# Kernel optimization log

Measured on AMD Instinct MI355X. Metric: run time of the kernel, lower is better.

Reference implementation:

```python
import jax, jax.numpy as jnp
import numpy as np

H, HK, D = 16, 4, 128          # query heads, kv heads, head_dim
HID, INTER = 2048, 8192        # hidden_size, intermediate_size
L, N_UND = 4096, 3072          # total packed len (sum(sample_lens)), num und tokens
SAMPLE_LENS = [2048, 2048]
EPS = 1e-6


def rmsnorm(x, w, eps=EPS):
    v = jnp.mean(jnp.square(x), axis=-1, keepdims=True)
    return x * jax.lax.rsqrt(v + eps) * w


def setup_inputs() -> dict:
    key = jax.random.key(0)
    ks = jax.random.split(key, 12)
    x = jax.random.normal(ks[0], (N_UND, HID), jnp.float32)
    und_idx = jnp.sort(jax.random.permutation(ks[1], L)[:N_UND]).astype(jnp.int64)
    # RoPE tables (source computes RoPE but its attention consumes pre-RoPE tensors)
    pos = jnp.arange(L, dtype=jnp.float32)
    inv_freq = 1.0 / (10000.0 ** (jnp.arange(0, D, 2, dtype=jnp.float32) / D))
    ang = pos[:, None] * inv_freq[None, :]
    cos = jnp.concatenate([jnp.cos(ang), jnp.cos(ang)], axis=-1)
    sin = jnp.concatenate([jnp.sin(ang), jnp.sin(ang)], axis=-1)
    # block-diagonal causal mask over packed sequence (one causal block per sample)
    offs = np.cumsum([0] + SAMPLE_LENS)
    m = np.zeros((L, L), dtype=bool)
    for a, b in zip(offs[:-1], offs[1:]):
        m[a:b, a:b] = np.tril(np.ones((b - a, b - a), dtype=bool))
    mask = jnp.asarray(m)
    w = lambda k, shape: jax.random.normal(k, shape, jnp.float32) * 0.02
    return dict(
        packed_sequence=x, und_idx=und_idx, cos=cos, sin=sin, mask=mask,
        Wq=w(ks[2], (H * D, HID)), bq=w(ks[3], (H * D,)),
        Wk=w(ks[4], (HK * D, HID)), bk=w(ks[5], (HK * D,)),
        Wv=w(ks[6], (HK * D, HID)), bv=w(ks[7], (HK * D,)),
        Wo=w(ks[8], (HID, H * D)),
        q_norm_w=jnp.ones((D,), jnp.float32), k_norm_w=jnp.ones((D,), jnp.float32),
        ln1_w=jnp.ones((HID,), jnp.float32), ln2_w=jnp.ones((HID,), jnp.float32),
        Wg=w(ks[9], (INTER, HID)), Wu=w(ks[10], (INTER, HID)), Wd=w(ks[11], (HID, INTER)),
    )


def reference(packed_sequence, und_idx, cos, sin, mask, Wq, bq, Wk, bk, Wv, bv, Wo,
              q_norm_w, k_norm_w, ln1_w, ln2_w, Wg, Wu, Wd):
    G = H // HK  # num_key_value_groups
    resid = packed_sequence
    x = rmsnorm(packed_sequence, ln1_w)
    # projections on und tokens only, then scatter into zero-initialized packed tensors
    q = (x @ Wq.T + bq).reshape(-1, H, D)
    k = (x @ Wk.T + bk).reshape(-1, HK, D)
    v = (x @ Wv.T + bv).reshape(-1, HK, D)
    Q = jnp.zeros((L, H, D), x.dtype).at[und_idx].set(q)
    K = jnp.zeros((L, HK, D), x.dtype).at[und_idx].set(k)
    V = jnp.zeros((L, HK, D), x.dtype).at[und_idx].set(v)
    # QK RMSNorm (zero rows stay zero, matching scatter-of-normed-und-rows)
    Q = rmsnorm(Q, q_norm_w)
    K = rmsnorm(K, k_norm_w)
    # NOTE: the source applies apply_rotary_pos_emb(Q, K, cos, sin) but both attention
    # branches consume the pre-RoPE normed tensors, so RoPE has no effect; we mirror that.
    Kx = jnp.repeat(K, G, axis=1)  # [L, H, D] GQA expand (each kv head repeated G times)
    Vx = jnp.repeat(V, G, axis=1)
    scores = jnp.einsum('qhd,khd->hqk', Q, Kx) / jnp.sqrt(jnp.asarray(D, x.dtype))
    scores = jnp.where(mask[None], scores, jnp.finfo(scores.dtype).min)
    attn = jax.nn.softmax(scores, axis=-1)
    ctx = jnp.einsum('hqk,khd->qhd', attn, Vx).reshape(L, H * D)
    attn_out = ctx[und_idx] @ Wo.T
    h = resid + attn_out
    y = rmsnorm(h, ln2_w)
    mlp = (jax.nn.silu(y @ Wg.T) * (y @ Wu.T)) @ Wd.T
    return h + mlp
```

## Files before the change

### kernel.cpp

```cpp
#include <hip/hip_runtime.h>
#include <math.h>


#define NU     3072
#define LPACK  4096
#define HIDN   2048
#define QKV_LD 3072
#define EPSF   1e-6f

typedef unsigned short u16;
typedef unsigned int   u32;
typedef __attribute__((ext_vector_type(8)))  __bf16 bf16x8;
typedef __attribute__((ext_vector_type(4)))  float  f32x4;
typedef __attribute__((ext_vector_type(16))) float  f32x16;

union FRAG { uint4 q; u16 u[8]; bf16x8 b; };

__device__ __forceinline__ u16 f2bf(float f) {
    u32 u = __float_as_uint(f);
    u32 r = (u + 0x7fffu + ((u >> 16) & 1u)) >> 16;
    return (u16)r;
}
__device__ __forceinline__ float bf2f(u16 h) {
    return __uint_as_float(((u32)h) << 16);
}
__device__ __forceinline__ void gload_lds16(const u16* g, u16* lds) {
    __builtin_amdgcn_global_load_lds(
        (const __attribute__((address_space(1))) u32*)g,
        (__attribute__((address_space(3))) u32*)lds, 16, 0, 0);
}


__global__ __launch_bounds__(256) void inv_init_kernel(int* __restrict__ inv) {
    inv[blockIdx.x * 256 + threadIdx.x] = -1;
}
__global__ __launch_bounds__(256) void inv_set_kernel(const int* __restrict__ und,
                                                      int* __restrict__ inv) {
    int i = blockIdx.x * 256 + threadIdx.x;
    inv[und[i]] = i;
}


__global__ __launch_bounds__(256) void cvt_bf16_kernel(const float* __restrict__ in,
                                                       u16* __restrict__ out, int n8) {
    int idx = blockIdx.x * 256 + threadIdx.x;
    int stride = gridDim.x * 256;
    for (int i = idx; i < n8; i += stride) {
        float4 a = *(const float4*)(in + (size_t)i * 8);
        float4 b = *(const float4*)(in + (size_t)i * 8 + 4);
        FRAG f;
        f.u[0] = f2bf(a.x); f.u[1] = f2bf(a.y); f.u[2] = f2bf(a.z); f.u[3] = f2bf(a.w);
        f.u[4] = f2bf(b.x); f.u[5] = f2bf(b.y); f.u[6] = f2bf(b.z); f.u[7] = f2bf(b.w);
        *(uint4*)(out + (size_t)i * 8) = f.q;
    }
}


__global__ __launch_bounds__(256) void rmsnorm_bf16_kernel(const float* __restrict__ in,
                                                           const float* __restrict__ w,
                                                           u16* __restrict__ out) {
    int row = blockIdx.x;
    const float4* p = (const float4*)(in + (size_t)row * HIDN);
    float4 a = p[threadIdx.x * 2];
    float4 b = p[threadIdx.x * 2 + 1];
    float ss = a.x*a.x + a.y*a.y + a.z*a.z + a.w*a.w
             + b.x*b.x + b.y*b.y + b.z*b.z + b.w*b.w;
    #pragma unroll
    for (int off = 32; off > 0; off >>= 1) ss += __shfl_xor(ss, off, 64);
    __shared__ float red[4];
    if ((threadIdx.x & 63) == 0) red[threadIdx.x >> 6] = ss;
    __syncthreads();
    float tot = red[0] + red[1] + red[2] + red[3];
    float sc  = rsqrtf(tot * (1.0f / HIDN) + EPSF);
    const float4* wp = (const float4*)w;
    float4 w0 = wp[threadIdx.x * 2], w1 = wp[threadIdx.x * 2 + 1];
    FRAG f;
    f.u[0] = f2bf(a.x*sc*w0.x); f.u[1] = f2bf(a.y*sc*w0.y);
    f.u[2] = f2bf(a.z*sc*w0.z); f.u[3] = f2bf(a.w*sc*w0.w);
    f.u[4] = f2bf(b.x*sc*w1.x); f.u[5] = f2bf(b.y*sc*w1.y);
    f.u[6] = f2bf(b.z*sc*w1.z); f.u[7] = f2bf(b.w*sc*w1.w);
    *(uint4*)(out + (size_t)row * HIDN + threadIdx.x * 8) = f.q;
}


__global__ __launch_bounds__(64) void qnorm_kernel(u16* __restrict__ qkv,
                                                   const float* __restrict__ w) {
    int i = blockIdx.x, h = blockIdx.y, t = threadIdx.x;
    u16* p = qkv + (size_t)i * QKV_LD + h * 128 + t * 2;
    u32 pr = *(u32*)p;
    float x0 = bf2f((u16)(pr & 0xffff)), x1 = bf2f((u16)(pr >> 16));
    float ss = x0*x0 + x1*x1;
    #pragma unroll
    for (int off = 32; off > 0; off >>= 1) ss += __shfl_xor(ss, off, 64);
    float sc = rsqrtf(ss * (1.0f / 128.f) + EPSF);
    float2 wv = *(const float2*)(w + t * 2);
    u32 res = (u32)f2bf(x0*sc*wv.x) | ((u32)f2bf(x1*sc*wv.y) << 16);
    *(u32*)p = res;
}


__global__ __launch_bounds__(64) void scatter_kv_kernel(const u16* __restrict__ qkvb,
                                                        const int* __restrict__ inv,
                                                        const float* __restrict__ knw,
                                                        u16* __restrict__ Kb,
                                                        u16* __restrict__ Vb) {
    int l = blockIdx.x, hkk = blockIdx.y, t = threadIdx.x;
    int i = inv[l];
    size_t off = (size_t)l * 512 + hkk * 128 + t * 2;
    if (i < 0) {
        *(u32*)(Kb + off) = 0u;
        *(u32*)(Vb + off) = 0u;
        return;
    }
    const u16* kp = qkvb + (size_t)i * QKV_LD + 2048 + hkk * 128 + t * 2;
    u32 kv = *(const u32*)kp;
    float k0 = bf2f((u16)(kv & 0xffff)), k1 = bf2f((u16)(kv >> 16));
    float ss = k0*k0 + k1*k1;
    #pragma unroll
    for (int off2 = 32; off2 > 0; off2 >>= 1) ss += __shfl_xor(ss, off2, 64);
    float sc = rsqrtf(ss * (1.0f / 128.f) + EPSF);
    float2 wv = *(const float2*)(knw + t * 2);
    u32 res = (u32)f2bf(k0*sc*wv.x) | ((u32)f2bf(k1*sc*wv.y) << 16);
    *(u32*)(Kb + off) = res;
    const u16* vp = qkvb + (size_t)i * QKV_LD + 2560 + hkk * 128 + t * 2;
    *(u32*)(Vb + off) = *(const u32*)vp;
}


template <int MODE>
__global__ __launch_bounds__(256, 2) void gemm_bf16_kernel(
        const u16* __restrict__ A, int lda,
        const u16* __restrict__ B0, const u16* __restrict__ B1, const u16* __restrict__ B2,
        int n1, int n2, int ldb,
        const float* __restrict__ bias0, const float* __restrict__ bias1,
        const float* __restrict__ bias2,
        const float* __restrict__ addend,
        void* __restrict__ Cout, int ldc, int K)
{
    __shared__ u16 As[128 * 64];
    __shared__ u16 Bs[128 * 64];
    const int tid = threadIdx.x;
    const int w = tid >> 6, lane = tid & 63;
    const int m0 = blockIdx.y * 128, n0 = blockIdx.x * 128;
    const u16* Bp; const float* bias; int nb;
    if (n0 < n1)      { Bp = B0; bias = bias0; nb = n0; }
    else if (n0 < n2) { Bp = B1; bias = bias1; nb = n0 - n1; }
    else              { Bp = B2; bias = bias2; nb = n0 - n2; }
    const int wr = w >> 1, wc = w & 1;
    const int cl = lane & 15, kg = lane >> 4;

    f32x4 acc[4][4];
    #pragma unroll
    for (int i = 0; i < 4; ++i)
        #pragma unroll
        for (int j = 0; j < 4; ++j)
            #pragma unroll
            for (int r = 0; r < 4; ++r) acc[i][j][r] = 0.f;

    for (int k0 = 0; k0 < K; k0 += 64) {
        #pragma unroll
        for (int j = 0; j < 4; ++j) {
            int slot = j * 256 + tid;
            int row = slot >> 3, jp = slot & 7;
            int j2 = jp ^ (row & 7);
            gload_lds16(A + (size_t)(m0 + row) * lda + k0 + j2 * 8,
                        &As[(j * 256 + w * 64) * 8]);
        }
        #pragma unroll
        for (int j = 0; j < 4; ++j) {
            int slot = j * 256 + tid;
            int row = slot >> 3, jp = slot & 7;
            int j2 = jp ^ (row & 7);
            gload_lds16(Bp + (size_t)(nb + row) * ldb + k0 + j2 * 8,
                        &Bs[(j * 256 + w * 64) * 8]);
        }
        __syncthreads();
        #pragma unroll
        for (int ks = 0; ks < 2; ++ks) {
            FRAG af[4], bfr[4];
            #pragma unroll
            for (int mi = 0; mi < 4; ++mi) {
                int row = wr * 64 + mi * 16 + cl;
                int dblk = ks * 4 + kg;
                af[mi].q = *(const uint4*)&As[row * 64 + ((dblk ^ (row & 7)) * 8)];
            }
            #pragma unroll
            for (int ni = 0; ni < 4; ++ni) {
                int row = wc * 64 + ni * 16 + cl;
                int dblk = ks * 4 + kg;
                bfr[ni].q = *(const uint4*)&Bs[row * 64 + ((dblk ^ (row & 7)) * 8)];
            }
            #pragma unroll
            for (int mi = 0; mi < 4; ++mi)
                #pragma unroll
                for (int ni = 0; ni < 4; ++ni)
                    acc[mi][ni] = __builtin_amdgcn_mfma_f32_16x16x32_bf16(
                        af[mi].b, bfr[ni].b, acc[mi][ni], 0, 0, 0);
        }
        __syncthreads();
    }
    #pragma unroll
    for (int mi = 0; mi < 4; ++mi) {
        #pragma unroll
        for (int ni = 0; ni < 4; ++ni) {
            int gcol = n0 + wc * 64 + ni * 16 + cl;
            float bv = 0.f;
            if (MODE == 0) bv = bias[nb + wc * 64 + ni * 16 + cl];
            #pragma unroll
            for (int r = 0; r < 4; ++r) {
                int grow = m0 + wr * 64 + mi * 16 + kg * 4 + r;
                float v = acc[mi][ni][r] + bv;
                if (MODE == 0) {
                    ((u16*)Cout)[(size_t)grow * ldc + gcol] = f2bf(v);
                } else {
                    v += addend[(size_t)grow * ldc + gcol];
                    ((float*)Cout)[(size_t)grow * ldc + gcol] = v;
                }
            }
        }
    }
}


__global__ __launch_bounds__(256, 2) void gemm_gateup_bf16_kernel(
        const u16* __restrict__ A,
        const u16* __restrict__ Bg, const u16* __restrict__ Bu,
        u16* __restrict__ act, int ldc)
{
    __shared__ u16 As[128 * 64];
    __shared__ u16 Gs[128 * 64];
    __shared__ u16 Us[128 * 64];
    const int tid = threadIdx.x;
    const int w = tid >> 6, lane = tid & 63;
    const int m0 = blockIdx.y * 128, n0 = blockIdx.x * 128;
    const int wr = w >> 1, wc = w & 1;
    const int cl = lane & 15, kg = lane >> 4;

    f32x4 ag[4][4], au[4][4];
    #pragma unroll
    for (int i = 0; i < 4; ++i)
        #pragma unroll
        for (int j = 0; j < 4; ++j)
            #pragma unroll
            for (int r = 0; r < 4; ++r) { ag[i][j][r] = 0.f; au[i][j][r] = 0.f; }

    for (int k0 = 0; k0 < HIDN; k0 += 64) {
        #pragma unroll
        for (int j = 0; j < 4; ++j) {
            int slot = j * 256 + tid;
            int row = slot >> 3, jp = slot & 7;
            int j2 = jp ^ (row & 7);
            gload_lds16(A + (size_t)(m0 + row) * HIDN + k0 + j2 * 8,
                        &As[(j * 256 + w * 64) * 8]);
            gload_lds16(Bg + (size_t)(n0 + row) * HIDN + k0 + j2 * 8,
                        &Gs[(j * 256 + w * 64) * 8]);
            gload_lds16(Bu + (size_t)(n0 + row) * HIDN + k0 + j2 * 8,
                        &Us[(j * 256 + w * 64) * 8]);
        }
        __syncthreads();
        #pragma unroll
        for (int ks = 0; ks < 2; ++ks) {
            FRAG af[4], gf[4], uf[4];
            #pragma unroll
            for (int mi = 0; mi < 4; ++mi) {
                int row = wr * 64 + mi * 16 + cl;
                int dblk = ks * 4 + kg;
                af[mi].q = *(const uint4*)&As[row * 64 + ((dblk ^ (row & 7)) * 8)];
            }
            #pragma unroll
            for (int ni = 0; ni < 4; ++ni) {
                int row = wc * 64 + ni * 16 + cl;
                int dblk = ks * 4 + kg;
                gf[ni].q = *(const uint4*)&Gs[row * 64 + ((dblk ^ (row & 7)) * 8)];
                uf[ni].q = *(const uint4*)&Us[row * 64 + ((dblk ^ (row & 7)) * 8)];
            }
            #pragma unroll
            for (int mi = 0; mi < 4; ++mi)
                #pragma unroll
                for (int ni = 0; ni < 4; ++ni) {
                    ag[mi][ni] = __builtin_amdgcn_mfma_f32_16x16x32_bf16(
                        af[mi].b, gf[ni].b, ag[mi][ni], 0, 0, 0);
                    au[mi][ni] = __builtin_amdgcn_mfma_f32_16x16x32_bf16(
                        af[mi].b, uf[ni].b, au[mi][ni], 0, 0, 0);
                }
        }
        __syncthreads();
    }
    #pragma unroll
    for (int mi = 0; mi < 4; ++mi) {
        #pragma unroll
        for (int ni = 0; ni < 4; ++ni) {
            int gcol = n0 + wc * 64 + ni * 16 + cl;
            #pragma unroll
            for (int r = 0; r < 4; ++r) {
                int grow = m0 + wr * 64 + mi * 16 + kg * 4 + r;
                float g = ag[mi][ni][r], u = au[mi][ni][r];
                float s = g / (1.f + __expf(-g));
                act[(size_t)grow * ldc + gcol] = f2bf(s * u);
            }
        }
    }
}


__global__ __launch_bounds__(256, 2) void attn_mfma_kernel(
        const u16* __restrict__ qkv,
        const u16* __restrict__ Kb,
        const u16* __restrict__ Vb,
        const int* __restrict__ und,
        u16* __restrict__ ctxb)
{
    const int h = blockIdx.y, hk = h >> 2;
    const int i0 = blockIdx.x * 128;
    const int tid = threadIdx.x;
    const int w = tid >> 6, lane = tid & 63;
    const int ql = lane & 31, hi = lane >> 5;

    __shared__ u16  Kt[32 * 128];
    __shared__ u16  Vt[128 * 40];
    __shared__ float Ot[4][32][36];

    const int iq  = i0 + w * 32 + ql;
    const int pqv = und[iq];
    const int rsv = pqv & ~2047;
    const int kend_w = __shfl(pqv, 31, 64);
    const int kbeg_w = __shfl(pqv, 0, 64) & ~2047;
    const int kbeg_b = und[i0] & ~2047;
    const int kend_b = und[i0 + 127];

    FRAG qf[8];
    const u16* qbase = qkv + (size_t)iq * QKV_LD + h * 128;
    #pragma unroll
    for (int ds = 0; ds < 8; ++ds)
        qf[ds].q = *(const uint4*)(qbase + ds * 16 + hi * 8);

    f32x16 Oa[4];
    #pragma unroll
    for (int dg = 0; dg < 4; ++dg)
        #pragma unroll
        for (int r = 0; r < 16; ++r) Oa[dg][r] = 0.f;
    float m_run = -1e30f, l_run = 0.f;
    const float SCALE = 0.08838834764831845f;

    for (int k0 = kbeg_b; k0 <= kend_b; k0 += 32) {
        #pragma unroll
        for (int j = 0; j < 2; ++j) {
            int sb = (j * 4 + w) * 64;
            int slot = sb + lane;
            int r = slot >> 4, jp = slot & 15;
            int jj = jp ^ (r & 15);
            gload_lds16(Kb + (size_t)(k0 + r) * 512 + hk * 128 + jj * 8, &Kt[sb * 8]);
        }
        {
            int kp = tid & 15, d0 = (tid >> 4) * 8;
            const u16* v0 = Vb + (size_t)(k0 + kp * 2) * 512 + hk * 128 + d0;
            FRAG r0, r1;
            r0.q = *(const uint4*)v0;
            r1.q = *(const uint4*)(v0 + 512);
            #pragma unroll
            for (int i = 0; i < 8; ++i) {
                u32 val = (u32)r0.u[i] | ((u32)r1.u[i] << 16);
                *(u32*)&Vt[(d0 + i) * 40 + kp * 2] = val;
            }
        }
        __syncthreads();
        if (k0 + 31 >= kbeg_w && k0 <= kend_w) {
            f32x16 st;
            #pragma unroll
            for (int r = 0; r < 16; ++r) st[r] = 0.f;
            #pragma unroll
            for (int ds = 0; ds < 8; ++ds) {
                FRAG kf;
                kf.q = *(const uint4*)&Kt[ql * 128 + (((ds * 2 + hi) ^ (ql & 15)) * 8)];
                st = __builtin_amdgcn_mfma_f32_32x32x16_bf16(kf.b, qf[ds].b, st, 0, 0, 0);
            }
            float p[16];
            float mloc = -1e30f;
            #pragma unroll
            for (int r = 0; r < 16; ++r) {
                int key = k0 + (r & 3) + ((r >> 2) << 3) + (hi << 2);
                float s = (key >= rsv && key <= pqv) ? st[r] * SCALE : -1e30f;
                p[r] = s;
                mloc = fmaxf(mloc, s);
            }
            float mfull = fmaxf(mloc, __shfl_xor(mloc, 32, 64));
            float mnew = fmaxf(m_run, mfull);
            float corr = __expf(m_run - mnew);
            float psum = 0.f;
            #pragma unroll
            for (int r = 0; r < 16; ++r) {
                float e = (p[r] > -1e29f) ? __expf(p[r] - mnew) : 0.f;
                p[r] = e; psum += e;
            }
            psum += __shfl_xor(psum, 32, 64);
            l_run = l_run * corr + psum;
            if (__any(mnew > m_run)) {
                #pragma unroll
                for (int r = 0; r < 16; ++r) {
                    float cr = __shfl(corr, (r & 3) + ((r >> 2) << 3) + (hi << 2), 64);
                    #pragma unroll
                    for (int dg = 0; dg < 4; ++dg) Oa[dg][r] *= cr;
                }
            }
            m_run = mnew;
            u32 pa[2][4];
            #pragma unroll
            for (int s = 0; s < 2; ++s) {
                #pragma unroll
                for (int t = 0; t < 2; ++t) {
                    u32 a = (u32)f2bf(p[8*s + 2*t]) | ((u32)f2bf(p[8*s + 2*t + 1]) << 16);
                    u32 b = (u32)f2bf(p[8*s + 4 + 2*t]) | ((u32)f2bf(p[8*s + 4 + 2*t + 1]) << 16);
                    asm volatile("v_permlane32_swap_b32 %0, %1" : "+v"(a), "+v"(b));
                    pa[s][t] = a; pa[s][t + 2] = b;
                }
            }
            #pragma unroll
            for (int s = 0; s < 2; ++s) {
                FRAG pau;
                pau.q = make_uint4(pa[s][0], pa[s][1], pa[s][2], pa[s][3]);
                #pragma unroll
                for (int dg = 0; dg < 4; ++dg) {
                    FRAG vf;
                    vf.q = *(const uint4*)&Vt[(dg * 32 + ql) * 40 + s * 16 + hi * 8];
                    Oa[dg] = __builtin_amdgcn_mfma_f32_32x32x16_bf16(pau.b, vf.b, Oa[dg], 0, 0, 0);
                }
            }
        }
        __syncthreads();
    }
    float linv = 1.f / l_run;
    #pragma unroll
    for (int dg = 0; dg < 4; ++dg) {
        #pragma unroll
        for (int r = 0; r < 16; ++r)
            Ot[w][(r & 3) + ((r >> 2) << 3) + (hi << 2)][ql] = Oa[dg][r];
        __syncthreads();
        float4 v0 = *(const float4*)&Ot[w][ql][hi * 16 + 0];
        float4 v1 = *(const float4*)&Ot[w][ql][hi * 16 + 4];
        float4 v2 = *(const float4*)&Ot[w][ql][hi * 16 + 8];
        float4 v3 = *(const float4*)&Ot[w][ql][hi * 16 + 12];
        FRAG a, b;
        a.u[0] = f2bf(v0.x * linv); a.u[1] = f2bf(v0.y * linv);
        a.u[2] = f2bf(v0.z * linv); a.u[3] = f2bf(v0.w * linv);
        a.u[4] = f2bf(v1.x * linv); a.u[5] = f2bf(v1.y * linv);
        a.u[6] = f2bf(v1.z * linv); a.u[7] = f2bf(v1.w * linv);
        b.u[0] = f2bf(v2.x * linv); b.u[1] = f2bf(v2.y * linv);
        b.u[2] = f2bf(v2.z * linv); b.u[3] = f2bf(v2.w * linv);
        b.u[4] = f2bf(v3.x * linv); b.u[5] = f2bf(v3.y * linv);
        b.u[6] = f2bf(v3.z * linv); b.u[7] = f2bf(v3.w * linv);
        u16* dst = ctxb + (size_t)(i0 + w * 32 + ql) * HIDN + h * 128 + dg * 32 + hi * 16;
        *(uint4*)dst = a.q;
        *(uint4*)(dst + 8) = b.q;
        __syncthreads();
    }
}


extern "C" void kernel_launch(void* const* d_in, const int* in_sizes, int n_in,
                              void* d_out, int out_size, void* d_ws, size_t ws_size,
                              hipStream_t stream) {
    const float* x    = (const float*)d_in[0];
    const int*   und  = (const int*)d_in[1];
    const float* Wq  = (const float*)d_in[5];
    const float* bq  = (const float*)d_in[6];
    const float* Wk  = (const float*)d_in[7];
    const float* bk  = (const float*)d_in[8];
    const float* Wv  = (const float*)d_in[9];
    const float* bv  = (const float*)d_in[10];
    const float* Wo  = (const float*)d_in[11];
    const float* qnw = (const float*)d_in[12];
    const float* knw = (const float*)d_in[13];
    const float* ln1 = (const float*)d_in[14];
    const float* ln2 = (const float*)d_in[15];
    const float* Wg  = (const float*)d_in[16];
    const float* Wu  = (const float*)d_in[17];
    const float* Wd  = (const float*)d_in[18];
    float* out = (float*)d_out;

    char* W = (char*)d_ws;
    u16* WqB = (u16*)(W + 0);
    u16* WkB = (u16*)(W + 8388608);
    u16* WvB = (u16*)(W + 10485760);
    u16* WoB = (u16*)(W + 12582912);
    u16* WgB = (u16*)(W + 20971520);
    u16* WuB = (u16*)(W + 54525952);
    u16* WdB = (u16*)(W + 88080384);
    char* R1 = W + 121634816;
    u16* qkvb = (u16*)R1;
    u16* ctxb = (u16*)(R1 + 18874368);
    u16* acth = (u16*)R1;
    float* hbuf = (float*)(W + 153092096);
    u16* xnb = (u16*)(W + 178257920);
    u16* Kbf = xnb;
    u16* Vbf = (u16*)(W + 178257920 + 4194304);
    u16* ynb = xnb;
    int* inv = (int*)(W + 190840832);

    const int BIG = 1 << 30;

    inv_init_kernel<<<16, 256, 0, stream>>>(inv);
    inv_set_kernel<<<12, 256, 0, stream>>>(und, inv);

    cvt_bf16_kernel<<<2048, 256, 0, stream>>>(Wq, WqB, 524288);
    cvt_bf16_kernel<<<512,  256, 0, stream>>>(Wk, WkB, 131072);
    cvt_bf16_kernel<<<512,  256, 0, stream>>>(Wv, WvB, 131072);
    cvt_bf16_kernel<<<2048, 256, 0, stream>>>(Wo, WoB, 524288);
    cvt_bf16_kernel<<<4096, 256, 0, stream>>>(Wg, WgB, 2097152);
    cvt_bf16_kernel<<<4096, 256, 0, stream>>>(Wu, WuB, 2097152);
    cvt_bf16_kernel<<<4096, 256, 0, stream>>>(Wd, WdB, 2097152);

    rmsnorm_bf16_kernel<<<NU, 256, 0, stream>>>(x, ln1, xnb);
    gemm_bf16_kernel<0><<<dim3(24, 24), 256, 0, stream>>>(
        xnb, 2048, WqB, WkB, WvB, 2048, 2560, 2048,
        bq, bk, bv, nullptr, qkvb, QKV_LD, 2048);
    qnorm_kernel<<<dim3(NU, 16), 64, 0, stream>>>(qkvb, qnw);
    scatter_kv_kernel<<<dim3(LPACK, 4), 64, 0, stream>>>(qkvb, inv, knw, Kbf, Vbf);
    attn_mfma_kernel<<<dim3(24, 16), 256, 0, stream>>>(qkvb, Kbf, Vbf, und, ctxb);
    gemm_bf16_kernel<1><<<dim3(16, 24), 256, 0, stream>>>(
        ctxb, 2048, WoB, WoB, WoB, BIG, BIG, 2048,
        nullptr, nullptr, nullptr, x, hbuf, 2048, 2048);
    rmsnorm_bf16_kernel<<<NU, 256, 0, stream>>>(hbuf, ln2, ynb);
    gemm_gateup_bf16_kernel<<<dim3(32, 24), 256, 0, stream>>>(
        ynb, WgB, WuB, acth, 4096);
    gemm_bf16_kernel<1><<<dim3(16, 24), 256, 0, stream>>>(
        acth, 4096, WdB, WdB, WdB, BIG, BIG, 8192,
        nullptr, nullptr, nullptr, hbuf, out, 2048, 4096);
    gemm_gateup_bf16_kernel<<<dim3(32, 24), 256, 0, stream>>>(
        ynb, WgB + (size_t)4096 * 2048, WuB + (size_t)4096 * 2048, acth, 4096);
    gemm_bf16_kernel<1><<<dim3(16, 24), 256, 0, stream>>>(
        acth, 4096, WdB + 4096, WdB, WdB, BIG, BIG, 8192,
        nullptr, nullptr, nullptr, out, out, 2048, 4096);
}
```

Baseline: 735.0 us.

## Split attention key range across wave pairs and merge softmax partials in LDS

The attention kernel now handles 64 queries per block instead of 128, with two wave pairs each walking half of the key tiles (split-K style). The partial max, sum and output of the two halves are merged through shared memory before the bf16 write, and the grid is doubled. This targets poor occupancy and load imbalance from the causal key range, since only 384 blocks previously ran long serial loops on 256 CUs. It also raises wave priority around the MFMA sections. The cost is a larger LDS footprint (36KB), an extra merge step, and K/V tiles that are no longer shared across all four waves.

```diff
diff --git a/kernel.cpp b/kernel.cpp
--- a/kernel.cpp
+++ b/kernel.cpp
@@ -311,22 +311,30 @@
         u16* __restrict__ ctxb)
 {
     const int h = blockIdx.y, hk = h >> 2;
-    const int i0 = blockIdx.x * 128;
+    const int i0 = blockIdx.x * 64;
     const int tid = threadIdx.x;
     const int w = tid >> 6, lane = tid & 63;
     const int ql = lane & 31, hi = lane >> 5;
-
-    __shared__ u16  Kt[32 * 128];
-    __shared__ u16  Vt[128 * 40];
-    __shared__ float Ot[4][32][36];
-
-    const int iq  = i0 + w * 32 + ql;
+    const int qsub = w & 1, kh = w >> 1;
+    const int tid2 = qsub * 64 + lane;
+
+    __shared__ __align__(16) unsigned char SM[36864];
+    u16*  Kt = (u16*)SM;
+    u16*  Vt = (u16*)(SM + 16384);
+    float* mM = (float*)SM;
+    float* mL = (float*)(SM + 512);
+    float* Om = (float*)(SM + 1024);
+    float* Ot = (float*)(SM + 9216);
+
+    const int iq  = i0 + qsub * 32 + ql;
     const int pqv = und[iq];
     const int rsv = pqv & ~2047;
     const int kend_w = __shfl(pqv, 31, 64);
     const int kbeg_w = __shfl(pqv, 0, 64) & ~2047;
     const int kbeg_b = und[i0] & ~2047;
-    const int kend_b = und[i0 + 127];
+    const int kend_b = und[i0 + 63];
+    const int ntiles = ((kend_b - kbeg_b) >> 5) + 1;
+    const int nhalf  = (ntiles + 1) >> 1;
 
     FRAG qf[8];
     const u16* qbase = qkv + (size_t)iq * QKV_LD + h * 128;
@@ -342,38 +350,48 @@
     float m_run = -1e30f, l_run = 0.f;
     const float SCALE = 0.08838834764831845f;
 
-    for (int k0 = kbeg_b; k0 <= kend_b; k0 += 32) {
-        #pragma unroll
-        for (int j = 0; j < 2; ++j) {
-            int sb = (j * 4 + w) * 64;
-            int slot = sb + lane;
-            int r = slot >> 4, jp = slot & 15;
-            int jj = jp ^ (r & 15);
-            gload_lds16(Kb + (size_t)(k0 + r) * 512 + hk * 128 + jj * 8, &Kt[sb * 8]);
-        }
-        {
-            int kp = tid & 15, d0 = (tid >> 4) * 8;
-            const u16* v0 = Vb + (size_t)(k0 + kp * 2) * 512 + hk * 128 + d0;
-            FRAG r0, r1;
-            r0.q = *(const uint4*)v0;
-            r1.q = *(const uint4*)(v0 + 512);
-            #pragma unroll
-            for (int i = 0; i < 8; ++i) {
-                u32 val = (u32)r0.u[i] | ((u32)r1.u[i] << 16);
-                *(u32*)&Vt[(d0 + i) * 40 + kp * 2] = val;
-            }
-        }
-        __syncthreads();
-        if (k0 + 31 >= kbeg_w && k0 <= kend_w) {
+    for (int it = 0; it < nhalf; ++it) {
+        const int t = kh ? (nhalf + it) : it;
+        const bool active = t < ntiles;
+        const int k0 = kbeg_b + (active ? t : 0) * 32;
+        if (active) {
+            #pragma unroll
+            for (int j = 0; j < 4; ++j) {
+                int slot = j * 128 + tid2;
+                int r = slot >> 4, jp = slot & 15;
+                int jj = jp ^ (r & 15);
+                gload_lds16(Kb + (size_t)(k0 + r) * 512 + hk * 128 + jj * 8,
+                            &Kt[kh * 4096 + (j * 128 + qsub * 64) * 8]);
+            }
+            int kp = tid2 & 15, d0 = (tid2 >> 4) * 8;
+            #pragma unroll
+            for (int h2 = 0; h2 < 2; ++h2) {
+                int dd = d0 + h2 * 64;
+                const u16* v0 = Vb + (size_t)(k0 + kp * 2) * 512 + hk * 128 + dd;
+                FRAG r0, r1;
+                r0.q = *(const uint4*)v0;
+                r1.q = *(const uint4*)(v0 + 512);
+                #pragma unroll
+                for (int i = 0; i < 8; ++i) {
+                    u32 val = (u32)r0.u[i] | ((u32)r1.u[i] << 16);
+                    *(u32*)&Vt[kh * 5120 + (dd + i) * 40 + kp * 2] = val;
+                }
+            }
+        }
+        __syncthreads();
+        if (active && k0 + 31 >= kbeg_w && k0 <= kend_w) {
             f32x16 st;
             #pragma unroll
             for (int r = 0; r < 16; ++r) st[r] = 0.f;
+            __builtin_amdgcn_s_setprio(1);
             #pragma unroll
             for (int ds = 0; ds < 8; ++ds) {
                 FRAG kf;
-                kf.q = *(const uint4*)&Kt[ql * 128 + (((ds * 2 + hi) ^ (ql & 15)) * 8)];
+                kf.q = *(const uint4*)&Kt[kh * 4096 + ql * 128 +
+                                          (((ds * 2 + hi) ^ (ql & 15)) * 8)];
                 st = __builtin_amdgcn_mfma_f32_32x32x16_bf16(kf.b, qf[ds].b, st, 0, 0, 0);
             }
+            __builtin_amdgcn_s_setprio(0);
             float p[16];
             float mloc = -1e30f;
             #pragma unroll
@@ -407,13 +425,14 @@
             #pragma unroll
             for (int s = 0; s < 2; ++s) {
                 #pragma unroll
-                for (int t = 0; t < 2; ++t) {
-                    u32 a = (u32)f2bf(p[8*s + 2*t]) | ((u32)f2bf(p[8*s + 2*t + 1]) << 16);
-                    u32 b = (u32)f2bf(p[8*s + 4 + 2*t]) | ((u32)f2bf(p[8*s + 4 + 2*t + 1]) << 16);
+                for (int t2 = 0; t2 < 2; ++t2) {
+                    u32 a = (u32)f2bf(p[8*s + 2*t2]) | ((u32)f2bf(p[8*s + 2*t2 + 1]) << 16);
+                    u32 b = (u32)f2bf(p[8*s + 4 + 2*t2]) | ((u32)f2bf(p[8*s + 4 + 2*t2 + 1]) << 16);
                     asm volatile("v_permlane32_swap_b32 %0, %1" : "+v"(a), "+v"(b));
-                    pa[s][t] = a; pa[s][t + 2] = b;
+                    pa[s][t2] = a; pa[s][t2 + 2] = b;
                 }
             }
+            __builtin_amdgcn_s_setprio(1);
             #pragma unroll
             for (int s = 0; s < 2; ++s) {
                 FRAG pau;
@@ -421,36 +440,70 @@
                 #pragma unroll
                 for (int dg = 0; dg < 4; ++dg) {
                     FRAG vf;
-                    vf.q = *(const uint4*)&Vt[(dg * 32 + ql) * 40 + s * 16 + hi * 8];
+                    vf.q = *(const uint4*)&Vt[kh * 5120 + (dg * 32 + ql) * 40 +
+                                              s * 16 + hi * 8];
                     Oa[dg] = __builtin_amdgcn_mfma_f32_32x32x16_bf16(pau.b, vf.b, Oa[dg], 0, 0, 0);
                 }
             }
-        }
-        __syncthreads();
-    }
-    float linv = 1.f / l_run;
+            __builtin_amdgcn_s_setprio(0);
+        }
+        __syncthreads();
+    }
+
+    if (hi == 0) {
+        mM[(kh * 2 + qsub) * 32 + ql] = m_run;
+        mL[(kh * 2 + qsub) * 32 + ql] = l_run;
+    }
+    __syncthreads();
+    float m0 = mM[qsub * 32 + ql],      l0 = mL[qsub * 32 + ql];
+    float m1 = mM[64 + qsub * 32 + ql], l1 = mL[64 + qsub * 32 + ql];
+    float mstar = fmaxf(m0, m1);
+    float f0 = __expf(m0 - mstar), f1 = __expf(m1 - mstar);
+    float lstar = f0 * l0 + f1 * l1;
+    float f_own = kh ? f1 : f0;
+    #pragma unroll
+    for (int r = 0; r < 16; ++r) {
+        float fr = __shfl(f_own, (r & 3) + ((r >> 2) << 3) + (hi << 2), 64);
+        #pragma unroll
+        for (int dg = 0; dg < 4; ++dg) Oa[dg][r] *= fr;
+    }
+    float linv = 1.f / lstar;
+
     #pragma unroll
     for (int dg = 0; dg < 4; ++dg) {
-        #pragma unroll
-        for (int r = 0; r < 16; ++r)
-            Ot[w][(r & 3) + ((r >> 2) << 3) + (hi << 2)][ql] = Oa[dg][r];
-        __syncthreads();
-        float4 v0 = *(const float4*)&Ot[w][ql][hi * 16 + 0];
-        float4 v1 = *(const float4*)&Ot[w][ql][hi * 16 + 4];
-        float4 v2 = *(const float4*)&Ot[w][ql][hi * 16 + 8];
-        float4 v3 = *(const float4*)&Ot[w][ql][hi * 16 + 12];
-        FRAG a, b;
-        a.u[0] = f2bf(v0.x * linv); a.u[1] = f2bf(v0.y * linv);
-        a.u[2] = f2bf(v0.z * linv); a.u[3] = f2bf(v0.w * linv);
-        a.u[4] = f2bf(v1.x * linv); a.u[5] = f2bf(v1.y * linv);
-        a.u[6] = f2bf(v1.z * linv); a.u[7] = f2bf(v1.w * linv);
-        b.u[0] = f2bf(v2.x * linv); b.u[1] = f2bf(v2.y * linv);
-        b.u[2] = f2bf(v2.z * linv); b.u[3] = f2bf(v2.w * linv);
-        b.u[4] = f2bf(v3.x * linv); b.u[5] = f2bf(v3.y * linv);
-        b.u[6] = f2bf(v3.z * linv); b.u[7] = f2bf(v3.w * linv);
-        u16* dst = ctxb + (size_t)(i0 + w * 32 + ql) * HIDN + h * 128 + dg * 32 + hi * 16;
-        *(uint4*)dst = a.q;
-        *(uint4*)(dst + 8) = b.q;
+        if (kh == 1) {
+            #pragma unroll
+            for (int r = 0; r < 16; ++r) {
+                int crow = (r & 3) + ((r >> 2) << 3) + (hi << 2);
+                Om[qsub * 1024 + crow * 32 + ql] = Oa[dg][r];
+            }
+        }
+        __syncthreads();
+        if (kh == 0) {
+            #pragma unroll
+            for (int r = 0; r < 16; ++r) {
+                int crow = (r & 3) + ((r >> 2) << 3) + (hi << 2);
+                float v = Oa[dg][r] + Om[qsub * 1024 + crow * 32 + ql];
+                Ot[qsub * 1152 + crow * 36 + ql] = v;
+            }
+            float4 v0 = *(const float4*)&Ot[qsub * 1152 + ql * 36 + hi * 16 + 0];
+            float4 v1 = *(const float4*)&Ot[qsub * 1152 + ql * 36 + hi * 16 + 4];
+            float4 v2 = *(const float4*)&Ot[qsub * 1152 + ql * 36 + hi * 16 + 8];
+            float4 v3 = *(const float4*)&Ot[qsub * 1152 + ql * 36 + hi * 16 + 12];
+            FRAG a, b;
+            a.u[0] = f2bf(v0.x * linv); a.u[1] = f2bf(v0.y * linv);
+            a.u[2] = f2bf(v0.z * linv); a.u[3] = f2bf(v0.w * linv);
+            a.u[4] = f2bf(v1.x * linv); a.u[5] = f2bf(v1.y * linv);
+            a.u[6] = f2bf(v1.z * linv); a.u[7] = f2bf(v1.w * linv);
+            b.u[0] = f2bf(v2.x * linv); b.u[1] = f2bf(v2.y * linv);
+            b.u[2] = f2bf(v2.z * linv); b.u[3] = f2bf(v2.w * linv);
+            b.u[4] = f2bf(v3.x * linv); b.u[5] = f2bf(v3.y * linv);
+            b.u[6] = f2bf(v3.z * linv); b.u[7] = f2bf(v3.w * linv);
+            u16* dst = ctxb + (size_t)(i0 + qsub * 32 + ql) * HIDN + h * 128 +
+                       dg * 32 + hi * 16;
+            *(uint4*)dst = a.q;
+            *(uint4*)(dst + 8) = b.q;
+        }
         __syncthreads();
     }
 }
@@ -515,7 +568,7 @@
         bq, bk, bv, nullptr, qkvb, QKV_LD, 2048);
     qnorm_kernel<<<dim3(NU, 16), 64, 0, stream>>>(qkvb, qnw);
     scatter_kv_kernel<<<dim3(LPACK, 4), 64, 0, stream>>>(qkvb, inv, knw, Kbf, Vbf);
-    attn_mfma_kernel<<<dim3(24, 16), 256, 0, stream>>>(qkvb, Kbf, Vbf, und, ctxb);
+    attn_mfma_kernel<<<dim3(48, 16), 256, 0, stream>>>(qkvb, Kbf, Vbf, und, ctxb);
     gemm_bf16_kernel<1><<<dim3(16, 24), 256, 0, stream>>>(
         ctxb, 2048, WoB, WoB, WoB, BIG, BIG, 2048,
         nullptr, nullptr, nullptr, x, hbuf, 2048, 2048);
```

Measured after the change: 751.4 us. +2.2%, slower.

## Double-buffer K/V tiles in attention and batch weight conversions into one launch

Applied to the files above, without the earlier changes.

The attention kernel now prefetches the next K tile into a second LDS buffer via global_load_lds and holds the next V tile in registers while the current tile is computed. This drops one barrier per iteration and hides load latency behind the MFMA work, and s_setprio raises wave priority around the MFMA sections. Shared memory is merged into one aliased byte buffer, so the epilogue reuses the K/V space. The seven weight-conversion launches become one 2D-grid kernel that reads per-segment arguments, cutting launch overhead at the cost of a fixed 1024-block grid per segment.

```diff
diff --git a/kernel.cpp b/kernel.cpp
--- a/kernel.cpp
+++ b/kernel.cpp
@@ -41,16 +41,25 @@
 }
 
 
-__global__ __launch_bounds__(256) void cvt_bf16_kernel(const float* __restrict__ in,
-                                                       u16* __restrict__ out, int n8) {
+struct CvtArgs {
+    const float* src[7];
+    u16*         dst[7];
+    int          n8[7];
+};
+
+__global__ __launch_bounds__(256) void cvt_all_kernel(CvtArgs a) {
+    int seg = blockIdx.y;
+    const float* in = a.src[seg];
+    u16* out = a.dst[seg];
+    int n8 = a.n8[seg];
     int idx = blockIdx.x * 256 + threadIdx.x;
     int stride = gridDim.x * 256;
     for (int i = idx; i < n8; i += stride) {
-        float4 a = *(const float4*)(in + (size_t)i * 8);
-        float4 b = *(const float4*)(in + (size_t)i * 8 + 4);
+        float4 va = *(const float4*)(in + (size_t)i * 8);
+        float4 vb = *(const float4*)(in + (size_t)i * 8 + 4);
         FRAG f;
-        f.u[0] = f2bf(a.x); f.u[1] = f2bf(a.y); f.u[2] = f2bf(a.z); f.u[3] = f2bf(a.w);
-        f.u[4] = f2bf(b.x); f.u[5] = f2bf(b.y); f.u[6] = f2bf(b.z); f.u[7] = f2bf(b.w);
+        f.u[0] = f2bf(va.x); f.u[1] = f2bf(va.y); f.u[2] = f2bf(va.z); f.u[3] = f2bf(va.w);
+        f.u[4] = f2bf(vb.x); f.u[5] = f2bf(vb.y); f.u[6] = f2bf(vb.z); f.u[7] = f2bf(vb.w);
         *(uint4*)(out + (size_t)i * 8) = f.q;
     }
 }
@@ -316,9 +325,10 @@
     const int w = tid >> 6, lane = tid & 63;
     const int ql = lane & 31, hi = lane >> 5;
 
-    __shared__ u16  Kt[32 * 128];
-    __shared__ u16  Vt[128 * 40];
-    __shared__ float Ot[4][32][36];
+    __shared__ __align__(16) unsigned char SM[36864];
+    u16*  Kt = (u16*)SM;
+    u16*  Vt = (u16*)(SM + 16384);
+    float* Ot = (float*)SM;
 
     const int iq  = i0 + w * 32 + ql;
     const int pqv = und[iq];
@@ -327,6 +337,7 @@
     const int kbeg_w = __shfl(pqv, 0, 64) & ~2047;
     const int kbeg_b = und[i0] & ~2047;
     const int kend_b = und[i0 + 127];
+    const int nt = ((kend_b - kbeg_b) >> 5) + 1;
 
     FRAG qf[8];
     const u16* qbase = qkv + (size_t)iq * QKV_LD + h * 128;
@@ -342,38 +353,61 @@
     float m_run = -1e30f, l_run = 0.f;
     const float SCALE = 0.08838834764831845f;
 
-    for (int k0 = kbeg_b; k0 <= kend_b; k0 += 32) {
+    const int kp = tid & 15, d0 = (tid >> 4) * 8;
+
+    FRAG vr0, vr1;
+    {
         #pragma unroll
         for (int j = 0; j < 2; ++j) {
             int sb = (j * 4 + w) * 64;
             int slot = sb + lane;
             int r = slot >> 4, jp = slot & 15;
             int jj = jp ^ (r & 15);
-            gload_lds16(Kb + (size_t)(k0 + r) * 512 + hk * 128 + jj * 8, &Kt[sb * 8]);
-        }
-        {
-            int kp = tid & 15, d0 = (tid >> 4) * 8;
-            const u16* v0 = Vb + (size_t)(k0 + kp * 2) * 512 + hk * 128 + d0;
-            FRAG r0, r1;
-            r0.q = *(const uint4*)v0;
-            r1.q = *(const uint4*)(v0 + 512);
-            #pragma unroll
-            for (int i = 0; i < 8; ++i) {
-                u32 val = (u32)r0.u[i] | ((u32)r1.u[i] << 16);
-                *(u32*)&Vt[(d0 + i) * 40 + kp * 2] = val;
-            }
-        }
-        __syncthreads();
+            gload_lds16(Kb + (size_t)(kbeg_b + r) * 512 + hk * 128 + jj * 8,
+                        &Kt[sb * 8]);
+        }
+        const u16* v0 = Vb + (size_t)(kbeg_b + kp * 2) * 512 + hk * 128 + d0;
+        vr0.q = *(const uint4*)v0;
+        vr1.q = *(const uint4*)(v0 + 512);
+    }
+
+    for (int t = 0; t < nt; ++t) {
+        const int cur = t & 1;
+        const int k0 = kbeg_b + t * 32;
+        #pragma unroll
+        for (int i = 0; i < 8; ++i) {
+            u32 val = (u32)vr0.u[i] | ((u32)vr1.u[i] << 16);
+            *(u32*)&Vt[cur * 5120 + (d0 + i) * 40 + kp * 2] = val;
+        }
+        __syncthreads();
+        if (t + 1 < nt) {
+            int kn = k0 + 32;
+            #pragma unroll
+            for (int j = 0; j < 2; ++j) {
+                int sb = (j * 4 + w) * 64;
+                int slot = sb + lane;
+                int r = slot >> 4, jp = slot & 15;
+                int jj = jp ^ (r & 15);
+                gload_lds16(Kb + (size_t)(kn + r) * 512 + hk * 128 + jj * 8,
+                            &Kt[(cur ^ 1) * 4096 + sb * 8]);
+            }
+            const u16* v0 = Vb + (size_t)(kn + kp * 2) * 512 + hk * 128 + d0;
+            vr0.q = *(const uint4*)v0;
+            vr1.q = *(const uint4*)(v0 + 512);
+        }
         if (k0 + 31 >= kbeg_w && k0 <= kend_w) {
             f32x16 st;
             #pragma unroll
             for (int r = 0; r < 16; ++r) st[r] = 0.f;
+            __builtin_amdgcn_s_setprio(1);
             #pragma unroll
             for (int ds = 0; ds < 8; ++ds) {
                 FRAG kf;
-                kf.q = *(const uint4*)&Kt[ql * 128 + (((ds * 2 + hi) ^ (ql & 15)) * 8)];
+                kf.q = *(const uint4*)&Kt[cur * 4096 + ql * 128 +
+                                          (((ds * 2 + hi) ^ (ql & 15)) * 8)];
                 st = __builtin_amdgcn_mfma_f32_32x32x16_bf16(kf.b, qf[ds].b, st, 0, 0, 0);
             }
+            __builtin_amdgcn_s_setprio(0);
             float p[16];
             float mloc = -1e30f;
             #pragma unroll
@@ -407,13 +441,14 @@
             #pragma unroll
             for (int s = 0; s < 2; ++s) {
                 #pragma unroll
-                for (int t = 0; t < 2; ++t) {
-                    u32 a = (u32)f2bf(p[8*s + 2*t]) | ((u32)f2bf(p[8*s + 2*t + 1]) << 16);
-                    u32 b = (u32)f2bf(p[8*s + 4 + 2*t]) | ((u32)f2bf(p[8*s + 4 + 2*t + 1]) << 16);
+                for (int t2 = 0; t2 < 2; ++t2) {
+                    u32 a = (u32)f2bf(p[8*s + 2*t2]) | ((u32)f2bf(p[8*s + 2*t2 + 1]) << 16);
+                    u32 b = (u32)f2bf(p[8*s + 4 + 2*t2]) | ((u32)f2bf(p[8*s + 4 + 2*t2 + 1]) << 16);
                     asm volatile("v_permlane32_swap_b32 %0, %1" : "+v"(a), "+v"(b));
-                    pa[s][t] = a; pa[s][t + 2] = b;
+                    pa[s][t2] = a; pa[s][t2 + 2] = b;
                 }
             }
+            __builtin_amdgcn_s_setprio(1);
             #pragma unroll
             for (int s = 0; s < 2; ++s) {
                 FRAG pau;
@@ -421,24 +456,27 @@
                 #pragma unroll
                 for (int dg = 0; dg < 4; ++dg) {
                     FRAG vf;
-                    vf.q = *(const uint4*)&Vt[(dg * 32 + ql) * 40 + s * 16 + hi * 8];
+                    vf.q = *(const uint4*)&Vt[cur * 5120 + (dg * 32 + ql) * 40 +
+                                              s * 16 + hi * 8];
                     Oa[dg] = __builtin_amdgcn_mfma_f32_32x32x16_bf16(pau.b, vf.b, Oa[dg], 0, 0, 0);
                 }
             }
-        }
-        __syncthreads();
-    }
+            __builtin_amdgcn_s_setprio(0);
+        }
+    }
+    __syncthreads();
+
     float linv = 1.f / l_run;
     #pragma unroll
     for (int dg = 0; dg < 4; ++dg) {
         #pragma unroll
         for (int r = 0; r < 16; ++r)
-            Ot[w][(r & 3) + ((r >> 2) << 3) + (hi << 2)][ql] = Oa[dg][r];
-        __syncthreads();
-        float4 v0 = *(const float4*)&Ot[w][ql][hi * 16 + 0];
-        float4 v1 = *(const float4*)&Ot[w][ql][hi * 16 + 4];
-        float4 v2 = *(const float4*)&Ot[w][ql][hi * 16 + 8];
-        float4 v3 = *(const float4*)&Ot[w][ql][hi * 16 + 12];
+            Ot[w * 1152 + ((r & 3) + ((r >> 2) << 3) + (hi << 2)) * 36 + ql] = Oa[dg][r];
+        __syncthreads();
+        float4 v0 = *(const float4*)&Ot[w * 1152 + ql * 36 + hi * 16 + 0];
+        float4 v1 = *(const float4*)&Ot[w * 1152 + ql * 36 + hi * 16 + 4];
+        float4 v2 = *(const float4*)&Ot[w * 1152 + ql * 36 + hi * 16 + 8];
+        float4 v3 = *(const float4*)&Ot[w * 1152 + ql * 36 + hi * 16 + 12];
         FRAG a, b;
         a.u[0] = f2bf(v0.x * linv); a.u[1] = f2bf(v0.y * linv);
         a.u[2] = f2bf(v0.z * linv); a.u[3] = f2bf(v0.w * linv);
@@ -501,13 +539,15 @@
     inv_init_kernel<<<16, 256, 0, stream>>>(inv);
     inv_set_kernel<<<12, 256, 0, stream>>>(und, inv);
 
-    cvt_bf16_kernel<<<2048, 256, 0, stream>>>(Wq, WqB, 524288);
-    cvt_bf16_kernel<<<512,  256, 0, stream>>>(Wk, WkB, 131072);
-    cvt_bf16_kernel<<<512,  256, 0, stream>>>(Wv, WvB, 131072);
-    cvt_bf16_kernel<<<2048, 256, 0, stream>>>(Wo, WoB, 524288);
-    cvt_bf16_kernel<<<4096, 256, 0, stream>>>(Wg, WgB, 2097152);
-    cvt_bf16_kernel<<<4096, 256, 0, stream>>>(Wu, WuB, 2097152);
-    cvt_bf16_kernel<<<4096, 256, 0, stream>>>(Wd, WdB, 2097152);
+    CvtArgs ca;
+    ca.src[0] = Wq; ca.dst[0] = WqB; ca.n8[0] = 524288;
+    ca.src[1] = Wk; ca.dst[1] = WkB; ca.n8[1] = 131072;
+    ca.src[2] = Wv; ca.dst[2] = WvB; ca.n8[2] = 131072;
+    ca.src[3] = Wo; ca.dst[3] = WoB; ca.n8[3] = 524288;
+    ca.src[4] = Wg; ca.dst[4] = WgB; ca.n8[4] = 2097152;
+    ca.src[5] = Wu; ca.dst[5] = WuB; ca.n8[5] = 2097152;
+    ca.src[6] = Wd; ca.dst[6] = WdB; ca.n8[6] = 2097152;
+    cvt_all_kernel<<<dim3(1024, 7), 256, 0, stream>>>(ca);
 
     rmsnorm_bf16_kernel<<<NU, 256, 0, stream>>>(x, ln1, xnb);
     gemm_bf16_kernel<0><<<dim3(24, 24), 256, 0, stream>>>(
```

Measured after the change: 733.2 us. About the same (-0.2%).
